# Performance work log

Hardware: AMD Instinct MI355X
Metric: run time of the kernel (lower is better)

The kernel has to match this reference:

```python
import jax, jax.numpy as jnp
import numpy as np

D_MODEL, H, D_FF = 1024, 16, 4096
D_K = D_MODEL // H
EPS = 1e-6
NEG = -1e9


def _layer_norm(x, alpha, bias):
    # torch LayerNormalization: scalar alpha/bias, unbiased std (ddof=1), eps added to std
    n = x.shape[-1]
    mu = jnp.mean(x, axis=-1, keepdims=True)
    var = jnp.sum((x - mu) ** 2, axis=-1, keepdims=True) / (n - 1)
    std = jnp.sqrt(var)
    return alpha * (x - mu) / (std + EPS) + bias


def _linear(x, w, b):
    # torch nn.Linear: y = x @ W^T + b, W: [out, in]
    return jnp.einsum('bsd,od->bso', x, w) + b


def setup_inputs() -> dict:
    key = jax.random.key(0)
    ks = jax.random.split(key, 12)
    d, dff = D_MODEL, D_FF
    s_d = 1.0 / np.sqrt(d)
    s_ff = 1.0 / np.sqrt(dff)
    inp = {
        'x': jax.random.normal(ks[0], (2, 2048, d), dtype=jnp.float32),
        'mask': jnp.ones((2, 1, 1, 2048), dtype=jnp.int32),
        'wq': jax.random.uniform(ks[1], (d, d), jnp.float32, -s_d, s_d),
        'bq': jnp.zeros((d,), jnp.float32),
        'wk': jax.random.uniform(ks[2], (d, d), jnp.float32, -s_d, s_d),
        'bk': jnp.zeros((d,), jnp.float32),
        'wv': jax.random.uniform(ks[3], (d, d), jnp.float32, -s_d, s_d),
        'bv': jnp.zeros((d,), jnp.float32),
        'wo': jax.random.uniform(ks[4], (d, d), jnp.float32, -s_d, s_d),
        'bo': jnp.zeros((d,), jnp.float32),
        'w1': jax.random.uniform(ks[5], (dff, d), jnp.float32, -s_d, s_d),
        'b1': jnp.zeros((dff,), jnp.float32),
        'w2': jax.random.uniform(ks[6], (d, dff), jnp.float32, -s_ff, s_ff),
        'b2': jnp.zeros((d,), jnp.float32),
        'ln1_a': jnp.ones((1,), jnp.float32),
        'ln1_b': jnp.zeros((1,), jnp.float32),
        'ln2_a': jnp.ones((1,), jnp.float32),
        'ln2_b': jnp.zeros((1,), jnp.float32),
    }
    return inp


def reference(x, mask, wq, bq, wk, bk, wv, bv, wo, bo, w1, b1, w2, b2,
              ln1_a, ln1_b, ln2_a, ln2_b):
    b, s, d = x.shape

    # --- residual 1: pre-norm self-attention (dropout is identity in eval) ---
    xn = _layer_norm(x, ln1_a, ln1_b)
    q = _linear(xn, wq, bq).reshape(b, s, H, D_K).transpose(0, 2, 1, 3)  # [b,h,s,dk]
    k = _linear(xn, wk, bk).reshape(b, s, H, D_K).transpose(0, 2, 1, 3)
    v = _linear(xn, wv, bv).reshape(b, s, H, D_K).transpose(0, 2, 1, 3)
    scores = jnp.einsum('bhqd,bhkd->bhqk', q, k) / jnp.sqrt(jnp.float32(D_K))
    scores = jnp.where(mask == 0, NEG, scores)
    p = jax.nn.softmax(scores, axis=-1)
    attn = jnp.einsum('bhqk,bhkd->bhqd', p, v)
    attn = attn.transpose(0, 2, 1, 3).reshape(b, s, d)
    x = x + _linear(attn, wo, bo)

    # --- residual 2: pre-norm feed-forward ---
    xn = _layer_norm(x, ln2_a, ln2_b)
    h = jax.nn.relu(_linear(xn, w1, b1))
    x = x + _linear(h, w2, b2)
    return x
```

## Files before the change

### kernel.cpp

```cpp
#include <hip/hip_runtime.h>
#include <hip/hip_bf16.h>
#include <stdint.h>

typedef __bf16 bf16x8 __attribute__((ext_vector_type(8)));
typedef __bf16 bf16x4 __attribute__((ext_vector_type(4)));
typedef short  s16x4  __attribute__((ext_vector_type(4)));
typedef float  f32x4  __attribute__((ext_vector_type(4)));
typedef unsigned short u16;

__device__ __forceinline__ u16 f2bf(float f) {
    return __builtin_bit_cast(u16, (__bf16)f);
}

__device__ __forceinline__ f32x4 vmax4(f32x4 a, f32x4 b) {
    f32x4 r;
    r[0] = fmaxf(a[0], b[0]); r[1] = fmaxf(a[1], b[1]);
    r[2] = fmaxf(a[2], b[2]); r[3] = fmaxf(a[3], b[3]);
    return r;
}
__device__ __forceinline__ f32x4 vexp4(f32x4 a) {
    f32x4 r;
    r[0] = __expf(a[0]); r[1] = __expf(a[1]);
    r[2] = __expf(a[2]); r[3] = __expf(a[3]);
    return r;
}

__device__ __forceinline__ f32x4 mfma16(bf16x4 a, bf16x4 b, f32x4 c) {
#if __has_builtin(__builtin_amdgcn_mfma_f32_16x16x16bf16_1k)
    return __builtin_amdgcn_mfma_f32_16x16x16bf16_1k(
        __builtin_bit_cast(s16x4, a), __builtin_bit_cast(s16x4, b), c, 0, 0, 0);
#else
    f32x4 d;
    asm volatile("v_mfma_f32_16x16x16_bf16 %0, %1, %2, %3"
                 : "=v"(d) : "v"(a), "v"(b), "v"(c));
    return d;
#endif
}

__device__ __forceinline__ void stage16(const void* g, void* lds_wave_base) {
#if __has_builtin(__builtin_amdgcn_global_load_lds)
    __builtin_amdgcn_global_load_lds(
        (const __attribute__((address_space(1))) void*)g,
        (__attribute__((address_space(3))) void*)lds_wave_base, 16, 0, 0);
#else
    int lane = threadIdx.x & 63;
    *(uint4*)((char*)lds_wave_base + lane * 16) = *(const uint4*)g;
#endif
}

__device__ __forceinline__ int swz(int r) {
    return (((r) & 7) ^ (((r) >> 3) & 7)) << 4;
}

__global__ void pack1_kernel(const float* __restrict__ wq, const float* __restrict__ wk,
                             const float* __restrict__ wv, const float* __restrict__ bq,
                             const float* __restrict__ bk, const float* __restrict__ bv,
                             const float* __restrict__ wo,
                             u16* __restrict__ wqkv, float* __restrict__ bqkv,
                             u16* __restrict__ wo_b) {
    size_t i0 = (size_t)blockIdx.x * 256 + threadIdx.x;
    size_t stride = (size_t)gridDim.x * 256;
    const size_t DD = 1024u * 1024u;
    for (size_t i = i0; i < 3 * DD; i += stride) {
        float v;
        if (i < DD)          v = wq[i] * 0.125f;
        else if (i < 2 * DD) v = wk[i - DD];
        else                 v = wv[i - 2 * DD];
        wqkv[i] = f2bf(v);
    }
    for (size_t i = i0; i < DD; i += stride) wo_b[i] = f2bf(wo[i]);
    for (size_t i = i0; i < 3072; i += stride)
        bqkv[i] = (i < 1024) ? bq[i] * 0.125f : ((i < 2048) ? bk[i - 1024] : bv[i - 2048]);
}

__global__ void pack2_kernel(const float* __restrict__ w1, const float* __restrict__ w2,
                             u16* __restrict__ w1_b, u16* __restrict__ w2_b) {
    size_t i0 = (size_t)blockIdx.x * 256 + threadIdx.x;
    size_t stride = (size_t)gridDim.x * 256;
    const size_t DD = 1024u * 1024u;
    for (size_t i = i0; i < 4 * DD; i += stride) w1_b[i] = f2bf(w1[i]);
    for (size_t i = i0; i < 4 * DD; i += stride) w2_b[i] = f2bf(w2[i]);
}

__global__ __launch_bounds__(256)
void ln_kernel(const float* __restrict__ x, u16* __restrict__ out,
               const float* __restrict__ alpha, const float* __restrict__ beta) {
    const int row = blockIdx.x;
    const int t = threadIdx.x, lane = t & 63, w = t >> 6;
    float4 v = ((const float4*)(x + (size_t)row * 1024))[t];
    float s  = v.x + v.y + v.z + v.w;
    float ss = v.x * v.x + v.y * v.y + v.z * v.z + v.w * v.w;
#pragma unroll
    for (int d = 1; d < 64; d <<= 1) { s += __shfl_xor(s, d); ss += __shfl_xor(ss, d); }
    __shared__ float red[8];
    if (lane == 0) { red[w] = s; red[4 + w] = ss; }
    __syncthreads();
    s  = red[0] + red[1] + red[2] + red[3];
    ss = red[4] + red[5] + red[6] + red[7];
    const float mu  = s * (1.f / 1024.f);
    const float var = fmaxf((ss - 1024.f * mu * mu) * (1.f / 1023.f), 0.f);
    const float inv = alpha[0] / (sqrtf(var) + 1e-6f);
    const float bb  = beta[0];
    ushort4 o;
    o.x = f2bf((v.x - mu) * inv + bb);
    o.y = f2bf((v.y - mu) * inv + bb);
    o.z = f2bf((v.z - mu) * inv + bb);
    o.w = f2bf((v.w - mu) * inv + bb);
    ((ushort4*)(out + (size_t)row * 1024))[t] = o;
}

template <int EPI>
__global__ __launch_bounds__(256)
void gemm_bt(const u16* __restrict__ A, const u16* __restrict__ B,
             const float* __restrict__ bias, const float* __restrict__ resid,
             void* __restrict__ Cout, int M, int N, int K, int ldc) {
    __shared__ __align__(16) char As[8192];
    __shared__ __align__(16) char Bs[8192];
    const int t = threadIdx.x;
    const int lane = t & 63, wave = t >> 6;
    const int g = lane >> 4, c = lane & 15;
    const int wm = wave >> 1, wn = wave & 1;
    const int bm = blockIdx.x, bn = blockIdx.y;

    const f32x4 z4 = {0.f, 0.f, 0.f, 0.f};
    f32x4 acc[4][4];
#pragma unroll
    for (int m = 0; m < 4; ++m)
#pragma unroll
        for (int n = 0; n < 4; ++n) acc[m][n] = z4;

    const int srow = t >> 2;
    const int ak = (((t & 3) ^ ((t >> 2) & 3)) << 3);
    const u16* ga = A + (size_t)(bm * 128 + srow) * K + ak;
    const u16* gb = B + (size_t)(bn * 128 + srow) * K + ak;
    char* la = As + wave * 1024;
    char* lb = Bs + wave * 1024;
    const size_t rstep = (size_t)64 * K;

    for (int k0 = 0; k0 < K; k0 += 32) {
        __syncthreads();
        stage16(ga + k0,         la);
        stage16(ga + k0 + rstep, la + 4096);
        stage16(gb + k0,         lb);
        stage16(gb + k0 + rstep, lb + 4096);
        __syncthreads();
        bf16x8 a[4], b[4];
#pragma unroll
        for (int m = 0; m < 4; ++m) {
            int r = wm * 64 + m * 16 + c;
            a[m] = *(const bf16x8*)(As + r * 64 + ((g * 16) ^ ((c & 3) << 4)));
        }
#pragma unroll
        for (int n = 0; n < 4; ++n) {
            int r = wn * 64 + n * 16 + c;
            b[n] = *(const bf16x8*)(Bs + r * 64 + ((g * 16) ^ ((c & 3) << 4)));
        }
#pragma unroll
        for (int m = 0; m < 4; ++m)
#pragma unroll
            for (int n = 0; n < 4; ++n)
                acc[m][n] = __builtin_amdgcn_mfma_f32_16x16x32_bf16(a[m], b[n], acc[m][n], 0, 0, 0);
    }

    const int row0 = bm * 128 + wm * 64;
    const int col0 = bn * 128 + wn * 64;
#pragma unroll
    for (int m = 0; m < 4; ++m) {
#pragma unroll
        for (int n = 0; n < 4; ++n) {
            const int cc = col0 + n * 16 + c;
            const float bv = bias[cc];
#pragma unroll
            for (int j = 0; j < 4; ++j) {
                const int rr = row0 + m * 16 + g * 4 + j;
                float v = acc[m][n][j] + bv;
                if (EPI == 1) v = v > 0.f ? v : 0.f;
                if (EPI == 2) {
                    ((float*)Cout)[(size_t)rr * ldc + cc] = resid[(size_t)rr * ldc + cc] + v;
                } else {
                    ((u16*)Cout)[(size_t)rr * ldc + cc] = f2bf(v);
                }
            }
        }
    }
}

__global__ __launch_bounds__(256)
void attn_kernel(const u16* __restrict__ qkv, const int* __restrict__ mask,
                 u16* __restrict__ attn_out) {
    __shared__ __align__(16) char Ksm[32768];
    __shared__ __align__(16) char Vsm[32768];
    const int t = threadIdx.x, lane = t & 63, w = t >> 6;
    const int g = lane >> 4, c = lane & 15;
    const int qt = blockIdx.x, h = blockIdx.y, b = blockIdx.z;
    const int S = 2048, LD = 3072;
    const int NT = S / 128;

    bf16x8 qf[2][2];
#pragma unroll
    for (int m = 0; m < 2; ++m)
#pragma unroll
        for (int half = 0; half < 2; ++half)
            qf[m][half] = *(const bf16x8*)&qkv[(size_t)(b * S + qt * 128 + w * 32 + m * 16 + c) * LD
                                               + h * 64 + half * 32 + g * 8];

    const f32x4 z4 = {0.f, 0.f, 0.f, 0.f};
    f32x4 accO[2][4];
#pragma unroll
    for (int m = 0; m < 2; ++m)
#pragma unroll
        for (int dt = 0; dt < 4; ++dt) accO[m][dt] = z4;
    float mrun[2] = {-1e30f, -1e30f};
    float lrun[2] = {0.f, 0.f};

    unsigned vr[2][8];
    const int vd0[2] = {((t) & 31) * 2, ((t) & 31) * 2};
    const int vkg[2] = {t >> 5, 8 + (t >> 5)};

    const int sk = (t * 2) >> 4;

    auto STAGEK = [&](int kt, char* Kd) {
#pragma unroll
        for (int it = 0; it < 4; ++it) {
            int idx = it * 256 + t;
            int k = idx >> 3, p = idx & 7;
            int ps = p ^ ((k & 7) ^ ((k >> 3) & 7));
            stage16(&qkv[(size_t)(b * S + kt * 128 + k) * LD + 1024 + h * 64 + ps * 8],
                    Kd + (it * 256 + w * 64) * 16);
        }
    };
    auto VLOAD = [&](int kt) {
#pragma unroll
        for (int it = 0; it < 2; ++it) {
            const u16* src = &qkv[(size_t)(b * S + kt * 128 + vkg[it] * 8) * LD + 2048 + h * 64 + vd0[it]];
#pragma unroll
            for (int i = 0; i < 8; ++i)
                vr[it][i] = *(const unsigned*)(src + (size_t)i * LD);
        }
    };
    auto VWRITE = [&](char* Vd) {
#pragma unroll
        for (int it = 0; it < 2; ++it) {
            int d0 = vd0[it], kg = vkg[it];
            uint4 lo, hi;
            lo.x = (vr[it][0] & 0xffffu) | (vr[it][1] << 16);
            lo.y = (vr[it][2] & 0xffffu) | (vr[it][3] << 16);
            lo.z = (vr[it][4] & 0xffffu) | (vr[it][5] << 16);
            lo.w = (vr[it][6] & 0xffffu) | (vr[it][7] << 16);
            hi.x = (vr[it][0] >> 16) | (vr[it][1] & 0xffff0000u);
            hi.y = (vr[it][2] >> 16) | (vr[it][3] & 0xffff0000u);
            hi.z = (vr[it][4] >> 16) | (vr[it][5] & 0xffff0000u);
            hi.w = (vr[it][6] >> 16) | (vr[it][7] & 0xffff0000u);
            *(uint4*)(Vd + d0 * 256 + ((kg * 16) ^ swz(d0)))       = lo;
            *(uint4*)(Vd + (d0 + 1) * 256 + ((kg * 16) ^ swz(d0 + 1))) = hi;
        }
    };

    STAGEK(0, Ksm);
    VLOAD(0);
    asm volatile("s_waitcnt vmcnt(0)" ::: "memory");
    VWRITE(Vsm);
    __syncthreads();

    int cur = 0;
    for (int kt = 0; kt < NT; ++kt) {
        char* Kc = Ksm + cur * 16384;
        char* Vc = Vsm + cur * 16384;
        if (kt + 1 < NT) {
            STAGEK(kt + 1, Ksm + (cur ^ 1) * 16384);
            VLOAD(kt + 1);
        }

        f32x4 s[2][8];
        __builtin_amdgcn_s_setprio(1);
#pragma unroll
        for (int n = 0; n < 8; ++n) {
            int kr = n * 16 + c;
            bf16x8 k0 = *(const bf16x8*)(Kc + kr * 128 + ((g * 16) ^ swz(kr)));
            bf16x8 k1 = *(const bf16x8*)(Kc + kr * 128 + ((64 + g * 16) ^ swz(kr)));
            s[0][n] = __builtin_amdgcn_mfma_f32_16x16x32_bf16(k0, qf[0][0], z4, 0, 0, 0);
            s[0][n] = __builtin_amdgcn_mfma_f32_16x16x32_bf16(k1, qf[0][1], s[0][n], 0, 0, 0);
            s[1][n] = __builtin_amdgcn_mfma_f32_16x16x32_bf16(k0, qf[1][0], z4, 0, 0, 0);
            s[1][n] = __builtin_amdgcn_mfma_f32_16x16x32_bf16(k1, qf[1][1], s[1][n], 0, 0, 0);
        }
        __builtin_amdgcn_s_setprio(0);
#pragma unroll
        for (int n = 0; n < 8; ++n) {
            int4 mv = *(const int4*)&mask[b * S + kt * 128 + n * 16 + g * 4];
            if (mv.x == 0) { s[0][n][0] = -1e9f; s[1][n][0] = -1e9f; }
            if (mv.y == 0) { s[0][n][1] = -1e9f; s[1][n][1] = -1e9f; }
            if (mv.z == 0) { s[0][n][2] = -1e9f; s[1][n][2] = -1e9f; }
            if (mv.w == 0) { s[0][n][3] = -1e9f; s[1][n][3] = -1e9f; }
        }
#pragma unroll
        for (int m = 0; m < 2; ++m) {
            f32x4 pm4 = s[m][0];
#pragma unroll
            for (int n = 1; n < 8; ++n) pm4 = vmax4(pm4, s[m][n]);
            float pm = fmaxf(fmaxf(pm4[0], pm4[1]), fmaxf(pm4[2], pm4[3]));
            pm = fmaxf(pm, __shfl_xor(pm, 16));
            pm = fmaxf(pm, __shfl_xor(pm, 32));
            float mn = fmaxf(mrun[m], pm);
            float sc = __expf(mrun[m] - mn);
            mrun[m] = mn;
            f32x4 mn4 = {mn, mn, mn, mn};
            f32x4 ps4 = z4;
#pragma unroll
            for (int n = 0; n < 8; ++n) { s[m][n] = vexp4(s[m][n] - mn4); ps4 += s[m][n]; }
            float ps = ps4[0] + ps4[1] + ps4[2] + ps4[3];
            ps += __shfl_xor(ps, 16);
            ps += __shfl_xor(ps, 32);
            lrun[m] = lrun[m] * sc + ps;
#pragma unroll
            for (int dt = 0; dt < 4; ++dt) accO[m][dt] *= sc;
        }
        __builtin_amdgcn_s_setprio(1);
#pragma unroll
        for (int n = 0; n < 8; ++n) {
            bf16x4 p0, p1;
#pragma unroll
            for (int j = 0; j < 4; ++j) { p0[j] = (__bf16)s[0][n][j]; p1[j] = (__bf16)s[1][n][j]; }
#pragma unroll
            for (int dt = 0; dt < 4; ++dt) {
                int d = dt * 16 + c;
                bf16x4 vf = *(const bf16x4*)(Vc + d * 256 + ((n * 32 + g * 8) ^ swz(d)));
                accO[0][dt] = mfma16(vf, p0, accO[0][dt]);
                accO[1][dt] = mfma16(vf, p1, accO[1][dt]);
            }
        }
        __builtin_amdgcn_s_setprio(0);

        asm volatile("s_waitcnt vmcnt(0)" ::: "memory");
        if (kt + 1 < NT) VWRITE(Vsm + (cur ^ 1) * 16384);
        __syncthreads();
        cur ^= 1;
    }

    char* Osm = Ksm;
#pragma unroll
    for (int m = 0; m < 2; ++m) {
        float inv = 1.f / lrun[m];
#pragma unroll
        for (int dt = 0; dt < 4; ++dt)
#pragma unroll
            for (int j = 0; j < 4; ++j) {
                int ql = w * 32 + m * 16 + c;
                int d = dt * 16 + g * 4 + j;
                *(u16*)(Osm + ql * 128 + ((d * 2) ^ swz(ql))) = f2bf(accO[m][dt][j] * inv);
            }
    }
    __syncthreads();
#pragma unroll
    for (int it = 0; it < 4; ++it) {
        int idx = it * 256 + t;
        int q = idx >> 3, p = idx & 7;
        uint4 val = *(const uint4*)(Osm + q * 128 + ((p * 16) ^ swz(q)));
        *(uint4*)&attn_out[(size_t)(b * S + qt * 128 + q) * 1024 + h * 64 + p * 8] = val;
    }
}

extern "C" void kernel_launch(void* const* d_in, const int* in_sizes, int n_in,
                              void* d_out, int out_size, void* d_ws, size_t ws_size,
                              hipStream_t stream) {
    const float* x    = (const float*)d_in[0];
    const int*   mask = (const int*)d_in[1];
    const float* wq   = (const float*)d_in[2];
    const float* bq   = (const float*)d_in[3];
    const float* wk   = (const float*)d_in[4];
    const float* bk   = (const float*)d_in[5];
    const float* wv   = (const float*)d_in[6];
    const float* bv   = (const float*)d_in[7];
    const float* wo   = (const float*)d_in[8];
    const float* bo   = (const float*)d_in[9];
    const float* w1   = (const float*)d_in[10];
    const float* b1   = (const float*)d_in[11];
    const float* w2   = (const float*)d_in[12];
    const float* b2   = (const float*)d_in[13];
    const float* ln1a = (const float*)d_in[14];
    const float* ln1b = (const float*)d_in[15];
    const float* ln2a = (const float*)d_in[16];
    const float* ln2b = (const float*)d_in[17];

    const size_t MB = 1048576;
    char* ws = (char*)d_ws;
    const bool big = ws_size >= 88 * MB;

    u16 *xn, *wqkv, *wo_b, *qkvb, *attnb, *w1_b, *w2_b, *hbuf;
    float *bqkv, *x1;
    int nchunk;
    if (big) {
        xn    = (u16*)(ws + 0 * MB);
        wqkv  = (u16*)(ws + 8 * MB);
        wo_b  = (u16*)(ws + 14 * MB);
        qkvb  = (u16*)(ws + 16 * MB);
        attnb = (u16*)(ws + 40 * MB);
        x1    = (float*)(ws + 48 * MB);
        w1_b  = (u16*)(ws + 64 * MB);
        w2_b  = (u16*)(ws + 72 * MB);
        hbuf  = (u16*)(ws + 16 * MB);
        bqkv  = (float*)(ws + 80 * MB);
        nchunk = 1;
    } else {
        xn    = (u16*)(ws + 0 * MB);
        wqkv  = (u16*)(ws + 8 * MB);
        wo_b  = (u16*)(ws + 14 * MB);
        qkvb  = (u16*)(ws + 16 * MB);
        attnb = (u16*)(ws + 40 * MB);
        x1    = (float*)(ws + 16 * MB);
        w1_b  = (u16*)(ws + 32 * MB);
        w2_b  = (u16*)(ws + 8 * MB);
        hbuf  = (u16*)(ws + 40 * MB);
        bqkv  = (float*)(ws + 40 * MB);
        nchunk = 4;
    }

    pack1_kernel<<<1024, 256, 0, stream>>>(wq, wk, wv, bq, bk, bv, wo, wqkv, bqkv, wo_b);
    ln_kernel<<<4096, 256, 0, stream>>>(x, xn, ln1a, ln1b);
    gemm_bt<0><<<dim3(32, 24), 256, 0, stream>>>(xn, wqkv, bqkv, nullptr, qkvb,
                                                 4096, 3072, 1024, 3072);
    attn_kernel<<<dim3(16, 16, 2), 256, 0, stream>>>(qkvb, mask, attnb);
    gemm_bt<2><<<dim3(32, 8), 256, 0, stream>>>(attnb, wo_b, bo, x, x1,
                                                4096, 1024, 1024, 1024);
    pack2_kernel<<<1024, 256, 0, stream>>>(w1, w2, w1_b, w2_b);
    ln_kernel<<<4096, 256, 0, stream>>>(x1, xn, ln2a, ln2b);

    const int mrows = 4096 / nchunk;
    for (int cidx = 0; cidx < nchunk; ++cidx) {
        const size_t ro = (size_t)cidx * mrows;
        gemm_bt<1><<<dim3(mrows / 128, 32), 256, 0, stream>>>(
            xn + ro * 1024, w1_b, b1, nullptr, hbuf, mrows, 4096, 1024, 4096);
        gemm_bt<2><<<dim3(mrows / 128, 8), 256, 0, stream>>>(
            hbuf, w2_b, b2, x1 + ro * 1024, (float*)d_out + ro * 1024,
            mrows, 1024, 4096, 1024);
    }
}
```

Measured before the change: 354.4 us.

## Use 512-thread attention blocks with one 16-row query tile per wave

The attention kernel now launches 512 threads (8 waves) per block instead of 256. Each wave handles 16 query rows rather than 32, so per-thread registers for scores, accumulators and V staging are halved. K/V staging work is spread over twice as many threads. The intent is more waves in flight and lower register pressure for better latency hiding. The cost is that each K/V fragment read from LDS feeds half as many MFMAs, and more waves share each block barrier.

```diff
diff --git a/kernel.cpp b/kernel.cpp
--- a/kernel.cpp
+++ b/kernel.cpp
@@ -185,7 +185,7 @@
     }
 }
 
-__global__ __launch_bounds__(256)
+__global__ __launch_bounds__(512)
 void attn_kernel(const u16* __restrict__ qkv, const int* __restrict__ mask,
                  u16* __restrict__ attn_out) {
     __shared__ __align__(16) char Ksm[32768];
@@ -196,64 +196,50 @@
     const int S = 2048, LD = 3072;
     const int NT = S / 128;
 
-    bf16x8 qf[2][2];
-#pragma unroll
-    for (int m = 0; m < 2; ++m)
-#pragma unroll
-        for (int half = 0; half < 2; ++half)
-            qf[m][half] = *(const bf16x8*)&qkv[(size_t)(b * S + qt * 128 + w * 32 + m * 16 + c) * LD
-                                               + h * 64 + half * 32 + g * 8];
+    bf16x8 qf[2];
+#pragma unroll
+    for (int half = 0; half < 2; ++half)
+        qf[half] = *(const bf16x8*)&qkv[(size_t)(b * S + qt * 128 + w * 16 + c) * LD
+                                        + h * 64 + half * 32 + g * 8];
 
     const f32x4 z4 = {0.f, 0.f, 0.f, 0.f};
-    f32x4 accO[2][4];
-#pragma unroll
-    for (int m = 0; m < 2; ++m)
-#pragma unroll
-        for (int dt = 0; dt < 4; ++dt) accO[m][dt] = z4;
-    float mrun[2] = {-1e30f, -1e30f};
-    float lrun[2] = {0.f, 0.f};
-
-    unsigned vr[2][8];
-    const int vd0[2] = {((t) & 31) * 2, ((t) & 31) * 2};
-    const int vkg[2] = {t >> 5, 8 + (t >> 5)};
-
-    const int sk = (t * 2) >> 4;
+    f32x4 accO[4];
+#pragma unroll
+    for (int dt = 0; dt < 4; ++dt) accO[dt] = z4;
+    float mrun = -1e30f, lrun = 0.f;
+
+    unsigned vr[8];
+    const int vd0 = (t & 31) * 2;
+    const int vkg = t >> 5;
 
     auto STAGEK = [&](int kt, char* Kd) {
 #pragma unroll
-        for (int it = 0; it < 4; ++it) {
-            int idx = it * 256 + t;
+        for (int it = 0; it < 2; ++it) {
+            int idx = it * 512 + t;
             int k = idx >> 3, p = idx & 7;
             int ps = p ^ ((k & 7) ^ ((k >> 3) & 7));
             stage16(&qkv[(size_t)(b * S + kt * 128 + k) * LD + 1024 + h * 64 + ps * 8],
-                    Kd + (it * 256 + w * 64) * 16);
+                    Kd + (it * 512 + w * 64) * 16);
         }
     };
     auto VLOAD = [&](int kt) {
-#pragma unroll
-        for (int it = 0; it < 2; ++it) {
-            const u16* src = &qkv[(size_t)(b * S + kt * 128 + vkg[it] * 8) * LD + 2048 + h * 64 + vd0[it]];
-#pragma unroll
-            for (int i = 0; i < 8; ++i)
-                vr[it][i] = *(const unsigned*)(src + (size_t)i * LD);
-        }
+        const u16* src = &qkv[(size_t)(b * S + kt * 128 + vkg * 8) * LD + 2048 + h * 64 + vd0];
+#pragma unroll
+        for (int i = 0; i < 8; ++i)
+            vr[i] = *(const unsigned*)(src + (size_t)i * LD);
     };
     auto VWRITE = [&](char* Vd) {
-#pragma unroll
-        for (int it = 0; it < 2; ++it) {
-            int d0 = vd0[it], kg = vkg[it];
-            uint4 lo, hi;
-            lo.x = (vr[it][0] & 0xffffu) | (vr[it][1] << 16);
-            lo.y = (vr[it][2] & 0xffffu) | (vr[it][3] << 16);
-            lo.z = (vr[it][4] & 0xffffu) | (vr[it][5] << 16);
-            lo.w = (vr[it][6] & 0xffffu) | (vr[it][7] << 16);
-            hi.x = (vr[it][0] >> 16) | (vr[it][1] & 0xffff0000u);
-            hi.y = (vr[it][2] >> 16) | (vr[it][3] & 0xffff0000u);
-            hi.z = (vr[it][4] >> 16) | (vr[it][5] & 0xffff0000u);
-            hi.w = (vr[it][6] >> 16) | (vr[it][7] & 0xffff0000u);
-            *(uint4*)(Vd + d0 * 256 + ((kg * 16) ^ swz(d0)))       = lo;
-            *(uint4*)(Vd + (d0 + 1) * 256 + ((kg * 16) ^ swz(d0 + 1))) = hi;
-        }
+        uint4 lo, hi;
+        lo.x = (vr[0] & 0xffffu) | (vr[1] << 16);
+        lo.y = (vr[2] & 0xffffu) | (vr[3] << 16);
+        lo.z = (vr[4] & 0xffffu) | (vr[5] << 16);
+        lo.w = (vr[6] & 0xffffu) | (vr[7] << 16);
+        hi.x = (vr[0] >> 16) | (vr[1] & 0xffff0000u);
+        hi.y = (vr[2] >> 16) | (vr[3] & 0xffff0000u);
+        hi.z = (vr[4] >> 16) | (vr[5] & 0xffff0000u);
+        hi.w = (vr[6] >> 16) | (vr[7] & 0xffff0000u);
+        *(uint4*)(Vd + vd0 * 256 + ((vkg * 16) ^ swz(vd0)))           = lo;
+        *(uint4*)(Vd + (vd0 + 1) * 256 + ((vkg * 16) ^ swz(vd0 + 1))) = hi;
     };
 
     STAGEK(0, Ksm);
@@ -271,61 +257,57 @@
             VLOAD(kt + 1);
         }
 
-        f32x4 s[2][8];
+        f32x4 s[8];
         __builtin_amdgcn_s_setprio(1);
 #pragma unroll
         for (int n = 0; n < 8; ++n) {
             int kr = n * 16 + c;
             bf16x8 k0 = *(const bf16x8*)(Kc + kr * 128 + ((g * 16) ^ swz(kr)));
             bf16x8 k1 = *(const bf16x8*)(Kc + kr * 128 + ((64 + g * 16) ^ swz(kr)));
-            s[0][n] = __builtin_amdgcn_mfma_f32_16x16x32_bf16(k0, qf[0][0], z4, 0, 0, 0);
-            s[0][n] = __builtin_amdgcn_mfma_f32_16x16x32_bf16(k1, qf[0][1], s[0][n], 0, 0, 0);
-            s[1][n] = __builtin_amdgcn_mfma_f32_16x16x32_bf16(k0, qf[1][0], z4, 0, 0, 0);
-            s[1][n] = __builtin_amdgcn_mfma_f32_16x16x32_bf16(k1, qf[1][1], s[1][n], 0, 0, 0);
+            s[n] = __builtin_amdgcn_mfma_f32_16x16x32_bf16(k0, qf[0], z4, 0, 0, 0);
+            s[n] = __builtin_amdgcn_mfma_f32_16x16x32_bf16(k1, qf[1], s[n], 0, 0, 0);
         }
         __builtin_amdgcn_s_setprio(0);
 #pragma unroll
         for (int n = 0; n < 8; ++n) {
             int4 mv = *(const int4*)&mask[b * S + kt * 128 + n * 16 + g * 4];
-            if (mv.x == 0) { s[0][n][0] = -1e9f; s[1][n][0] = -1e9f; }
-            if (mv.y == 0) { s[0][n][1] = -1e9f; s[1][n][1] = -1e9f; }
-            if (mv.z == 0) { s[0][n][2] = -1e9f; s[1][n][2] = -1e9f; }
-            if (mv.w == 0) { s[0][n][3] = -1e9f; s[1][n][3] = -1e9f; }
-        }
-#pragma unroll
-        for (int m = 0; m < 2; ++m) {
-            f32x4 pm4 = s[m][0];
-#pragma unroll
-            for (int n = 1; n < 8; ++n) pm4 = vmax4(pm4, s[m][n]);
+            if (mv.x == 0) s[n][0] = -1e9f;
+            if (mv.y == 0) s[n][1] = -1e9f;
+            if (mv.z == 0) s[n][2] = -1e9f;
+            if (mv.w == 0) s[n][3] = -1e9f;
+        }
+        {
+            f32x4 pm4 = s[0];
+#pragma unroll
+            for (int n = 1; n < 8; ++n) pm4 = vmax4(pm4, s[n]);
             float pm = fmaxf(fmaxf(pm4[0], pm4[1]), fmaxf(pm4[2], pm4[3]));
             pm = fmaxf(pm, __shfl_xor(pm, 16));
             pm = fmaxf(pm, __shfl_xor(pm, 32));
-            float mn = fmaxf(mrun[m], pm);
-            float sc = __expf(mrun[m] - mn);
-            mrun[m] = mn;
+            float mn = fmaxf(mrun, pm);
+            float sc = __expf(mrun - mn);
+            mrun = mn;
             f32x4 mn4 = {mn, mn, mn, mn};
             f32x4 ps4 = z4;
 #pragma unroll
-            for (int n = 0; n < 8; ++n) { s[m][n] = vexp4(s[m][n] - mn4); ps4 += s[m][n]; }
+            for (int n = 0; n < 8; ++n) { s[n] = vexp4(s[n] - mn4); ps4 += s[n]; }
             float ps = ps4[0] + ps4[1] + ps4[2] + ps4[3];
             ps += __shfl_xor(ps, 16);
             ps += __shfl_xor(ps, 32);
-            lrun[m] = lrun[m] * sc + ps;
-#pragma unroll
-            for (int dt = 0; dt < 4; ++dt) accO[m][dt] *= sc;
+            lrun = lrun * sc + ps;
+#pragma unroll
+            for (int dt = 0; dt < 4; ++dt) accO[dt] *= sc;
         }
         __builtin_amdgcn_s_setprio(1);
 #pragma unroll
         for (int n = 0; n < 8; ++n) {
-            bf16x4 p0, p1;
-#pragma unroll
-            for (int j = 0; j < 4; ++j) { p0[j] = (__bf16)s[0][n][j]; p1[j] = (__bf16)s[1][n][j]; }
+            bf16x4 p0;
+#pragma unroll
+            for (int j = 0; j < 4; ++j) p0[j] = (__bf16)s[n][j];
 #pragma unroll
             for (int dt = 0; dt < 4; ++dt) {
                 int d = dt * 16 + c;
                 bf16x4 vf = *(const bf16x4*)(Vc + d * 256 + ((n * 32 + g * 8) ^ swz(d)));
-                accO[0][dt] = mfma16(vf, p0, accO[0][dt]);
-                accO[1][dt] = mfma16(vf, p1, accO[1][dt]);
+                accO[dt] = mfma16(vf, p0, accO[dt]);
             }
         }
         __builtin_amdgcn_s_setprio(0);
@@ -337,22 +319,21 @@
     }
 
     char* Osm = Ksm;
-#pragma unroll
-    for (int m = 0; m < 2; ++m) {
-        float inv = 1.f / lrun[m];
+    {
+        float inv = 1.f / lrun;
+        int ql = w * 16 + c;
 #pragma unroll
         for (int dt = 0; dt < 4; ++dt)
 #pragma unroll
             for (int j = 0; j < 4; ++j) {
-                int ql = w * 32 + m * 16 + c;
                 int d = dt * 16 + g * 4 + j;
-                *(u16*)(Osm + ql * 128 + ((d * 2) ^ swz(ql))) = f2bf(accO[m][dt][j] * inv);
+                *(u16*)(Osm + ql * 128 + ((d * 2) ^ swz(ql))) = f2bf(accO[dt][j] * inv);
             }
     }
     __syncthreads();
 #pragma unroll
-    for (int it = 0; it < 4; ++it) {
-        int idx = it * 256 + t;
+    for (int it = 0; it < 2; ++it) {
+        int idx = it * 512 + t;
         int q = idx >> 3, p = idx & 7;
         uint4 val = *(const uint4*)(Osm + q * 128 + ((p * 16) ^ swz(q)));
         *(uint4*)&attn_out[(size_t)(b * S + qt * 128 + q) * 1024 + h * 64 + p * 8] = val;
@@ -418,7 +399,7 @@
     ln_kernel<<<4096, 256, 0, stream>>>(x, xn, ln1a, ln1b);
     gemm_bt<0><<<dim3(32, 24), 256, 0, stream>>>(xn, wqkv, bqkv, nullptr, qkvb,
                                                  4096, 3072, 1024, 3072);
-    attn_kernel<<<dim3(16, 16, 2), 256, 0, stream>>>(qkvb, mask, attnb);
+    attn_kernel<<<dim3(16, 16, 2), 512, 0, stream>>>(qkvb, mask, attnb);
     gemm_bt<2><<<dim3(32, 8), 256, 0, stream>>>(attnb, wo_b, bo, x, x1,
                                                 4096, 1024, 1024, 1024);
     pack2_kernel<<<1024, 256, 0, stream>>>(w1, w2, w1_b, w2_b);
```

After: 374.2 us. 5.6% more time.
